# Kernel tuning notes

Hardware: AMD Instinct MI355X
Metric: run time of the kernel (lower is better)

Reference implementation:

```python
import jax, jax.numpy as jnp
import numpy as np
from jax.scipy.special import logsumexp

D_MODEL = 512
NHEAD = 8
BATCH = 2
SEQ = 1024


def _safe_log_relu(v):
    # log(max(v, 0)) with well-defined (zero) gradient where v <= 0
    pos = v > 0
    return jnp.where(pos, jnp.log(jnp.where(pos, v, 1.0)), -jnp.inf)


def _split_heads(t, h):
    b, l, hd = t.shape
    return t.reshape(b, l, h, hd // h).transpose(0, 2, 1, 3)  # (B,H,L,d)


def setup_inputs() -> dict:
    key = jax.random.key(0)
    ks = jax.random.split(key, 9)
    s = 1.0 / np.sqrt(D_MODEL)
    x = jax.random.normal(ks[0], (BATCH, SEQ, D_MODEL), jnp.float32)
    mk = lambda k: jax.random.normal(k, (D_MODEL, D_MODEL), jnp.float32) * s
    mb = lambda k: jax.random.normal(k, (D_MODEL,), jnp.float32) * 0.02
    return {
        "x": x,
        "W_Q": mk(ks[1]), "b_Q": mb(ks[2]),
        "W_K": mk(ks[3]), "b_K": mb(ks[4]),
        "W_V": mk(ks[5]), "b_V": mb(ks[6]),
        "W_O": mk(ks[7]), "b_O": mb(ks[8]),
    }


def reference(x, W_Q, b_Q, W_K, b_K, W_V, b_V, W_O, b_O):
    # self-attention: queries = keys = values = x
    Q = _split_heads(x @ W_Q.T + b_Q, NHEAD)  # (B,H,L,D)
    K = _split_heads(x @ W_K.T + b_K, NHEAD)  # (B,H,L,D)
    V = _split_heads(x @ W_V.T + b_V, NHEAD)  # (B,H,L,Dv)

    # normalizer: log sum_j sum_d exp(Q_id) * exp(K_jd)
    log_B = logsumexp(Q + logsumexp(K, axis=-2, keepdims=True), axis=-1)  # (B,H,L)

    log_V_plus = _safe_log_relu(V)[..., None, :]    # (B,H,L,1,Dv)
    log_V_minus = _safe_log_relu(-V)[..., None, :]  # (B,H,L,1,Dv)

    # reduce over key positions: (B,H,L,D,Dv) -> (B,H,D,Dv)
    lse_KV_plus = logsumexp(K[..., :, :, None] + log_V_plus, axis=-3)
    lse_KV_minus = logsumexp(K[..., :, :, None] + log_V_minus, axis=-3)

    # reduce over feature dim D: (B,H,L,D,Dv) -> (B,H,L,Dv)
    log_A_plus = logsumexp(Q[..., None] + lse_KV_plus[..., None, :, :], axis=-2)
    log_A_minus = logsumexp(Q[..., None] + lse_KV_minus[..., None, :, :], axis=-2)

    heads = jnp.exp(log_A_plus - log_B[..., None]) - jnp.exp(log_A_minus - log_B[..., None])

    b, h, l, dv = heads.shape
    joined = heads.transpose(0, 2, 1, 3).reshape(b, l, h * dv)
    return joined @ W_O.T + b_O
```

## Files before the change

### kernel.cpp

```cpp
#include <hip/hip_runtime.h>
#include <math.h>

#define DM   512
#define NH   8
#define HD   64
#define B_   2
#define L_   1024
#define M_   (B_ * L_)

typedef __attribute__((ext_vector_type(8))) short  bfrag;
typedef __attribute__((ext_vector_type(4))) float  fv4;
typedef __attribute__((ext_vector_type(4))) unsigned short usv4;
typedef __attribute__((ext_vector_type(8))) unsigned short usv8;

__device__ __forceinline__ unsigned short f32_bf16_rne(float f) {
    unsigned u = __float_as_uint(f);
    unsigned r = u + 0x7FFF + ((u >> 16) & 1);
    return (unsigned short)(r >> 16);
}
__device__ __forceinline__ float bf16_f32(unsigned short h) {
    return __uint_as_float(((unsigned)h) << 16);
}

__global__ __launch_bounds__(256) void prep_kernel(
    const float* __restrict__ x,
    const float* __restrict__ Wq, const float* __restrict__ Wk,
    const float* __restrict__ Wv, const float* __restrict__ Wo,
    unsigned short* __restrict__ xh, unsigned short* __restrict__ xl,
    unsigned short* __restrict__ wh, unsigned short* __restrict__ wl) {
    int bid = blockIdx.x;
    const float* src; unsigned short *dh, *dl; size_t off;
    if (bid < 1024) {
        src = x; dh = xh; dl = xl; off = (size_t)bid * 1024;
    } else {
        int wsel = (bid - 1024) >> 8;
        int wb   = (bid - 1024) & 255;
        src = (wsel == 0) ? Wq : (wsel == 1) ? Wk : (wsel == 2) ? Wv : Wo;
        dh = wh + (size_t)wsel * 262144;
        dl = wl + (size_t)wsel * 262144;
        off = (size_t)wb * 1024;
    }
    size_t i = off + (size_t)threadIdx.x * 4;
    float4 v = *(const float4*)(src + i);
    usv4 h, l;
    h.x = f32_bf16_rne(v.x); l.x = f32_bf16_rne(v.x - bf16_f32(h.x));
    h.y = f32_bf16_rne(v.y); l.y = f32_bf16_rne(v.y - bf16_f32(h.y));
    h.z = f32_bf16_rne(v.z); l.z = f32_bf16_rne(v.z - bf16_f32(h.z));
    h.w = f32_bf16_rne(v.w); l.w = f32_bf16_rne(v.w - bf16_f32(h.w));
    *(usv4*)(dh + i) = h;
    *(usv4*)(dl + i) = l;
}

#define TM 128
#define TN 64
#define TK 32
#define LDA 40

__device__ __forceinline__ void mfma_gemm_bf16(
    const unsigned short* __restrict__ Ahg, const unsigned short* __restrict__ Alg,
    const unsigned short* __restrict__ Bhg, const unsigned short* __restrict__ Blg,
    const float* __restrict__ bias, float* __restrict__ C, int do_exp) {
    __shared__ __align__(16) unsigned short Ah[TM * LDA];
    __shared__ __align__(16) unsigned short Al[TM * LDA];
    __shared__ __align__(16) unsigned short Bh[TN * LDA];
    __shared__ __align__(16) unsigned short Bl[TN * LDA];

    const int tid  = threadIdx.x;
    const int wave = tid >> 6, lane = tid & 63;
    const int quad = lane >> 4, r16 = lane & 15;
    const int m0 = blockIdx.y * TM, n0 = blockIdx.x * TN;

    fv4 acc[2][4] = {};

    for (int k0 = 0; k0 < DM; k0 += TK) {
#pragma unroll
        for (int t = 0; t < 2; ++t) {
            int idx = tid + t * 256;
            int row = idx >> 2, ch = (idx & 3) << 3;
            size_t g = (size_t)(m0 + row) * DM + k0 + ch;
            *(usv8*)(Ah + row * LDA + ch) = *(const usv8*)(Ahg + g);
            *(usv8*)(Al + row * LDA + ch) = *(const usv8*)(Alg + g);
        }
        {
            int row = tid >> 2, ch = (tid & 3) << 3;
            size_t g = (size_t)(n0 + row) * DM + k0 + ch;
            *(usv8*)(Bh + row * LDA + ch) = *(const usv8*)(Bhg + g);
            *(usv8*)(Bl + row * LDA + ch) = *(const usv8*)(Blg + g);
        }
        __syncthreads();

        bfrag ah[2], al[2], bh[4], bl[4];
#pragma unroll
        for (int i = 0; i < 2; ++i) {
            int off = (wave * 32 + i * 16 + r16) * LDA + quad * 8;
            ah[i] = *(const bfrag*)(Ah + off);
            al[i] = *(const bfrag*)(Al + off);
        }
#pragma unroll
        for (int j = 0; j < 4; ++j) {
            int off = (j * 16 + r16) * LDA + quad * 8;
            bh[j] = *(const bfrag*)(Bh + off);
            bl[j] = *(const bfrag*)(Bl + off);
        }

#pragma unroll
        for (int i = 0; i < 2; ++i)
#pragma unroll
            for (int j = 0; j < 4; ++j) {
                acc[i][j] = __builtin_amdgcn_mfma_f32_16x16x32_bf16(ah[i], bh[j], acc[i][j], 0, 0, 0);
                acc[i][j] = __builtin_amdgcn_mfma_f32_16x16x32_bf16(ah[i], bl[j], acc[i][j], 0, 0, 0);
                acc[i][j] = __builtin_amdgcn_mfma_f32_16x16x32_bf16(al[i], bh[j], acc[i][j], 0, 0, 0);
            }
        __syncthreads();
    }

#pragma unroll
    for (int j = 0; j < 4; ++j) {
        int n = n0 + j * 16 + r16;
        float bn = bias[n];
#pragma unroll
        for (int i = 0; i < 2; ++i) {
#pragma unroll
            for (int r = 0; r < 4; ++r) {
                int m = m0 + wave * 32 + i * 16 + quad * 4 + r;
                float v = acc[i][j][r] + bn;
                if (do_exp) v = __expf(v);
                C[(size_t)m * DM + n] = v;
            }
        }
    }
}

__global__ __launch_bounds__(256) void gemm_qkv_kernel(
    const unsigned short* __restrict__ xh, const unsigned short* __restrict__ xl,
    const unsigned short* __restrict__ wh, const unsigned short* __restrict__ wl,
    const float* __restrict__ bq, const float* __restrict__ bk, const float* __restrict__ bv,
    float* __restrict__ Qe, float* __restrict__ Ke, float* __restrict__ V) {
    int z = blockIdx.z;
    const float* b = (z == 0) ? bq : (z == 1) ? bk : bv;
    float* C = (z == 0) ? Qe : (z == 1) ? Ke : V;
    mfma_gemm_bf16(xh, xl, wh + (size_t)z * 262144, wl + (size_t)z * 262144,
                   b, C, z < 2);
}

__global__ __launch_bounds__(256) void gemm_out_kernel(
    const unsigned short* __restrict__ jh, const unsigned short* __restrict__ jl,
    const unsigned short* __restrict__ wh, const unsigned short* __restrict__ wl,
    const float* __restrict__ bo, float* __restrict__ C) {
    mfma_gemm_bf16(jh, jl, wh + (size_t)3 * 262144, wl + (size_t)3 * 262144,
                   bo, C, 0);
}

#define JT 64
__global__ __launch_bounds__(256) void kv_stats_kernel(
    const float* __restrict__ Kbuf, const float* __restrict__ Vbuf,
    float* __restrict__ Spart, float* __restrict__ zpart) {
    const int split = blockIdx.x, bh = blockIdx.y;
    const int b = bh >> 3, h = bh & 7;
    const int j0 = split * JT;

    __shared__ float EK[JT][HD + 1];
    __shared__ float VS[JT][HD + 1];

    const int tid = threadIdx.x;
#pragma unroll
    for (int t = 0; t < 4; ++t) {
        int idx = tid + t * 256;
        int r = idx >> 4;
        int c = (idx & 15) << 2;
        size_t row = (size_t)(b * L_ + j0 + r) * DM + h * HD + c;
        float4 kv = *(const float4*)(Kbuf + row);
        EK[r][c + 0] = kv.x; EK[r][c + 1] = kv.y;
        EK[r][c + 2] = kv.z; EK[r][c + 3] = kv.w;
        float4 vv = *(const float4*)(Vbuf + row);
        VS[r][c + 0] = vv.x; VS[r][c + 1] = vv.y;
        VS[r][c + 2] = vv.z; VS[r][c + 3] = vv.w;
    }
    __syncthreads();

    const int tx = tid & 15, ty = tid >> 4;
    float acc[4][4] = {{0.f}};
#pragma unroll 8
    for (int jj = 0; jj < JT; ++jj) {
        float ek[4], vs[4];
#pragma unroll
        for (int i = 0; i < 4; ++i) ek[i] = EK[jj][ty * 4 + i];
#pragma unroll
        for (int j = 0; j < 4; ++j) vs[j] = VS[jj][tx * 4 + j];
#pragma unroll
        for (int i = 0; i < 4; ++i)
#pragma unroll
            for (int j = 0; j < 4; ++j) acc[i][j] += ek[i] * vs[j];
    }

    float* sp = Spart + ((size_t)bh * 16 + split) * (HD * HD);
#pragma unroll
    for (int i = 0; i < 4; ++i) {
        float4 o; o.x = acc[i][0]; o.y = acc[i][1]; o.z = acc[i][2]; o.w = acc[i][3];
        *(float4*)(sp + (ty * 4 + i) * HD + tx * 4) = o;
    }
    if (tid < HD) {
        float z = 0.f;
#pragma unroll 8
        for (int jj = 0; jj < JT; ++jj) z += EK[jj][tid];
        zpart[((size_t)bh * 16 + split) * HD + tid] = z;
    }
}

__global__ __launch_bounds__(256) void heads_kernel(
    const float* __restrict__ Qbuf, const float* __restrict__ Spart,
    const float* __restrict__ zpart,
    unsigned short* __restrict__ jh, unsigned short* __restrict__ jl) {
    const int tileI = blockIdx.x, bh = blockIdx.y;
    const int b = bh >> 3, h = bh & 7;

    __shared__ float S[HD][HD + 1];
    __shared__ float zl[HD];

    const int tid = threadIdx.x;
#pragma unroll
    for (int t = 0; t < 16; ++t) {
        int idx = tid + t * 256;
        float s = 0.f;
        const float* sp = Spart + (size_t)bh * 16 * (HD * HD) + idx;
#pragma unroll
        for (int p = 0; p < 16; ++p) s += sp[(size_t)p * (HD * HD)];
        S[idx >> 6][idx & 63] = s;
    }
    if (tid < HD) {
        float z = 0.f;
        const float* zp = zpart + (size_t)bh * 16 * HD + tid;
#pragma unroll
        for (int p = 0; p < 16; ++p) z += zp[(size_t)p * HD];
        zl[tid] = z;
    }
    __syncthreads();

    const int lane = tid & 63, w = tid >> 6;
#pragma unroll 1
    for (int r = 0; r < 16; ++r) {
        int i = tileI * 64 + w * 16 + r;
        float eq = Qbuf[(size_t)(b * L_ + i) * DM + h * HD + lane];

        float denom = eq * zl[lane];
#pragma unroll
        for (int off = 32; off; off >>= 1) denom += __shfl_xor(denom, off, 64);

        float acc = 0.f;
#pragma unroll
        for (int d = 0; d < HD; ++d) {
            float bq = __shfl(eq, d, 64);
            acc += bq * S[d][lane];
        }
        float val = acc / denom;
        size_t oidx = (size_t)(b * L_ + i) * DM + h * HD + lane;
        unsigned short hh = f32_bf16_rne(val);
        unsigned short ll = f32_bf16_rne(val - bf16_f32(hh));
        jh[oidx] = hh;
        jl[oidx] = ll;
    }
}

extern "C" void kernel_launch(void* const* d_in, const int* in_sizes, int n_in,
                              void* d_out, int out_size, void* d_ws, size_t ws_size,
                              hipStream_t stream) {
    const float* x  = (const float*)d_in[0];
    const float* Wq = (const float*)d_in[1];
    const float* bq = (const float*)d_in[2];
    const float* Wk = (const float*)d_in[3];
    const float* bk = (const float*)d_in[4];
    const float* Wv = (const float*)d_in[5];
    const float* bv = (const float*)d_in[6];
    const float* Wo = (const float*)d_in[7];
    const float* bo = (const float*)d_in[8];
    float* out = (float*)d_out;

    float* f = (float*)d_ws;
    const size_t NQ = (size_t)M_ * DM;
    float* Qe    = f;
    float* Ke    = f + NQ;
    float* V     = f + 2 * NQ;
    float* Spart = f + 3 * NQ;
    float* zpart = f + 4 * NQ;
    unsigned short* u = (unsigned short*)(f + 4 * NQ + 16384);
    unsigned short* xh = u;
    unsigned short* xl = u + NQ;
    unsigned short* wh = u + 2 * NQ;
    unsigned short* wl = u + 3 * NQ;
    unsigned short* jh = u + 4 * NQ;
    unsigned short* jl = u + 5 * NQ;

    prep_kernel<<<2048, 256, 0, stream>>>(x, Wq, Wk, Wv, Wo, xh, xl, wh, wl);

    dim3 gQKV(DM / TN, M_ / TM, 3);
    gemm_qkv_kernel<<<gQKV, 256, 0, stream>>>(xh, xl, wh, wl, bq, bk, bv, Qe, Ke, V);

    kv_stats_kernel<<<dim3(16, 16), 256, 0, stream>>>(Ke, V, Spart, zpart);

    heads_kernel<<<dim3(16, 16), 256, 0, stream>>>(Qe, Spart, zpart, jh, jl);

    dim3 gO(DM / TN, M_ / TM, 1);
    gemm_out_kernel<<<gO, 256, 0, stream>>>(jh, jl, wh, wl, bo, out);
}
```

Baseline: 142.5 us.

## Widen QKV GEMM N-tile and vectorize LDS accesses in stats kernels

After: 146.6 us. 1.03x slower.

```diff
diff --git a/kernel.cpp b/kernel.cpp
--- a/kernel.cpp
+++ b/kernel.cpp
@@ -52,25 +52,28 @@
 }
 
 #define TM 128
-#define TN 64
 #define TK 32
 #define LDA 40
 
+template <int TNv>
 __device__ __forceinline__ void mfma_gemm_bf16(
     const unsigned short* __restrict__ Ahg, const unsigned short* __restrict__ Alg,
     const unsigned short* __restrict__ Bhg, const unsigned short* __restrict__ Blg,
     const float* __restrict__ bias, float* __restrict__ C, int do_exp) {
+    constexpr int NF  = TNv / 16;
+    constexpr int BCH = TNv * 4 / 256;
+
     __shared__ __align__(16) unsigned short Ah[TM * LDA];
     __shared__ __align__(16) unsigned short Al[TM * LDA];
-    __shared__ __align__(16) unsigned short Bh[TN * LDA];
-    __shared__ __align__(16) unsigned short Bl[TN * LDA];
+    __shared__ __align__(16) unsigned short Bh[TNv * LDA];
+    __shared__ __align__(16) unsigned short Bl[TNv * LDA];
 
     const int tid  = threadIdx.x;
     const int wave = tid >> 6, lane = tid & 63;
     const int quad = lane >> 4, r16 = lane & 15;
-    const int m0 = blockIdx.y * TM, n0 = blockIdx.x * TN;
-
-    fv4 acc[2][4] = {};
+    const int m0 = blockIdx.y * TM, n0 = blockIdx.x * TNv;
+
+    fv4 acc[2][NF] = {};
 
     for (int k0 = 0; k0 < DM; k0 += TK) {
 #pragma unroll
@@ -81,15 +84,17 @@
             *(usv8*)(Ah + row * LDA + ch) = *(const usv8*)(Ahg + g);
             *(usv8*)(Al + row * LDA + ch) = *(const usv8*)(Alg + g);
         }
-        {
-            int row = tid >> 2, ch = (tid & 3) << 3;
+#pragma unroll
+        for (int t = 0; t < BCH; ++t) {
+            int idx = tid + t * 256;
+            int row = idx >> 2, ch = (idx & 3) << 3;
             size_t g = (size_t)(n0 + row) * DM + k0 + ch;
             *(usv8*)(Bh + row * LDA + ch) = *(const usv8*)(Bhg + g);
             *(usv8*)(Bl + row * LDA + ch) = *(const usv8*)(Blg + g);
         }
         __syncthreads();
 
-        bfrag ah[2], al[2], bh[4], bl[4];
+        bfrag ah[2], al[2], bh[NF], bl[NF];
 #pragma unroll
         for (int i = 0; i < 2; ++i) {
             int off = (wave * 32 + i * 16 + r16) * LDA + quad * 8;
@@ -97,7 +102,7 @@
             al[i] = *(const bfrag*)(Al + off);
         }
 #pragma unroll
-        for (int j = 0; j < 4; ++j) {
+        for (int j = 0; j < NF; ++j) {
             int off = (j * 16 + r16) * LDA + quad * 8;
             bh[j] = *(const bfrag*)(Bh + off);
             bl[j] = *(const bfrag*)(Bl + off);
@@ -106,7 +111,7 @@
 #pragma unroll
         for (int i = 0; i < 2; ++i)
 #pragma unroll
-            for (int j = 0; j < 4; ++j) {
+            for (int j = 0; j < NF; ++j) {
                 acc[i][j] = __builtin_amdgcn_mfma_f32_16x16x32_bf16(ah[i], bh[j], acc[i][j], 0, 0, 0);
                 acc[i][j] = __builtin_amdgcn_mfma_f32_16x16x32_bf16(ah[i], bl[j], acc[i][j], 0, 0, 0);
                 acc[i][j] = __builtin_amdgcn_mfma_f32_16x16x32_bf16(al[i], bh[j], acc[i][j], 0, 0, 0);
@@ -115,7 +120,7 @@
     }
 
 #pragma unroll
-    for (int j = 0; j < 4; ++j) {
+    for (int j = 0; j < NF; ++j) {
         int n = n0 + j * 16 + r16;
         float bn = bias[n];
 #pragma unroll
@@ -131,7 +136,7 @@
     }
 }
 
-__global__ __launch_bounds__(256) void gemm_qkv_kernel(
+__global__ __launch_bounds__(256, 2) void gemm_qkv_kernel(
     const unsigned short* __restrict__ xh, const unsigned short* __restrict__ xl,
     const unsigned short* __restrict__ wh, const unsigned short* __restrict__ wl,
     const float* __restrict__ bq, const float* __restrict__ bk, const float* __restrict__ bv,
@@ -139,16 +144,16 @@
     int z = blockIdx.z;
     const float* b = (z == 0) ? bq : (z == 1) ? bk : bv;
     float* C = (z == 0) ? Qe : (z == 1) ? Ke : V;
-    mfma_gemm_bf16(xh, xl, wh + (size_t)z * 262144, wl + (size_t)z * 262144,
-                   b, C, z < 2);
+    mfma_gemm_bf16<128>(xh, xl, wh + (size_t)z * 262144, wl + (size_t)z * 262144,
+                        b, C, z < 2);
 }
 
 __global__ __launch_bounds__(256) void gemm_out_kernel(
     const unsigned short* __restrict__ jh, const unsigned short* __restrict__ jl,
     const unsigned short* __restrict__ wh, const unsigned short* __restrict__ wl,
     const float* __restrict__ bo, float* __restrict__ C) {
-    mfma_gemm_bf16(jh, jl, wh + (size_t)3 * 262144, wl + (size_t)3 * 262144,
-                   bo, C, 0);
+    mfma_gemm_bf16<64>(jh, jl, wh + (size_t)3 * 262144, wl + (size_t)3 * 262144,
+                       bo, C, 0);
 }
 
 #define JT 64
@@ -159,8 +164,8 @@
     const int b = bh >> 3, h = bh & 7;
     const int j0 = split * JT;
 
-    __shared__ float EK[JT][HD + 1];
-    __shared__ float VS[JT][HD + 1];
+    __shared__ __align__(16) float EK[JT][HD + 4];
+    __shared__ __align__(16) float VS[JT][HD + 4];
 
     const int tid = threadIdx.x;
 #pragma unroll
@@ -170,11 +175,9 @@
         int c = (idx & 15) << 2;
         size_t row = (size_t)(b * L_ + j0 + r) * DM + h * HD + c;
         float4 kv = *(const float4*)(Kbuf + row);
-        EK[r][c + 0] = kv.x; EK[r][c + 1] = kv.y;
-        EK[r][c + 2] = kv.z; EK[r][c + 3] = kv.w;
+        *(float4*)&EK[r][c] = kv;
         float4 vv = *(const float4*)(Vbuf + row);
-        VS[r][c + 0] = vv.x; VS[r][c + 1] = vv.y;
-        VS[r][c + 2] = vv.z; VS[r][c + 3] = vv.w;
+        *(float4*)&VS[r][c] = vv;
     }
     __syncthreads();
 
@@ -182,15 +185,14 @@
     float acc[4][4] = {{0.f}};
 #pragma unroll 8
     for (int jj = 0; jj < JT; ++jj) {
-        float ek[4], vs[4];
-#pragma unroll
-        for (int i = 0; i < 4; ++i) ek[i] = EK[jj][ty * 4 + i];
-#pragma unroll
-        for (int j = 0; j < 4; ++j) vs[j] = VS[jj][tx * 4 + j];
+        float4 ek = *(const float4*)&EK[jj][ty * 4];
+        float4 vs = *(const float4*)&VS[jj][tx * 4];
+        float e[4] = {ek.x, ek.y, ek.z, ek.w};
+        float v[4] = {vs.x, vs.y, vs.z, vs.w};
 #pragma unroll
         for (int i = 0; i < 4; ++i)
 #pragma unroll
-            for (int j = 0; j < 4; ++j) acc[i][j] += ek[i] * vs[j];
+            for (int j = 0; j < 4; ++j) acc[i][j] += e[i] * v[j];
     }
 
     float* sp = Spart + ((size_t)bh * 16 + split) * (HD * HD);
@@ -214,18 +216,22 @@
     const int tileI = blockIdx.x, bh = blockIdx.y;
     const int b = bh >> 3, h = bh & 7;
 
-    __shared__ float S[HD][HD + 1];
+    __shared__ __align__(16) float S[HD][HD + 4];
     __shared__ float zl[HD];
 
     const int tid = threadIdx.x;
 #pragma unroll
-    for (int t = 0; t < 16; ++t) {
-        int idx = tid + t * 256;
-        float s = 0.f;
-        const float* sp = Spart + (size_t)bh * 16 * (HD * HD) + idx;
-#pragma unroll
-        for (int p = 0; p < 16; ++p) s += sp[(size_t)p * (HD * HD)];
-        S[idx >> 6][idx & 63] = s;
+    for (int t = 0; t < 4; ++t) {
+        int idx4 = tid + t * 256;
+        const float* sp = Spart + (size_t)bh * 16 * (HD * HD) + (size_t)idx4 * 4;
+        float4 s = {0.f, 0.f, 0.f, 0.f};
+#pragma unroll
+        for (int p = 0; p < 16; ++p) {
+            float4 v = *(const float4*)(sp + (size_t)p * (HD * HD));
+            s.x += v.x; s.y += v.y; s.z += v.z; s.w += v.w;
+        }
+        int row = idx4 >> 4, col = (idx4 & 15) << 2;
+        *(float4*)&S[row][col] = s;
     }
     if (tid < HD) {
         float z = 0.f;
@@ -292,13 +298,13 @@
 
     prep_kernel<<<2048, 256, 0, stream>>>(x, Wq, Wk, Wv, Wo, xh, xl, wh, wl);
 
-    dim3 gQKV(DM / TN, M_ / TM, 3);
+    dim3 gQKV(DM / 128, M_ / TM, 3);
     gemm_qkv_kernel<<<gQKV, 256, 0, stream>>>(xh, xl, wh, wl, bq, bk, bv, Qe, Ke, V);
 
     kv_stats_kernel<<<dim3(16, 16), 256, 0, stream>>>(Ke, V, Spart, zpart);
 
     heads_kernel<<<dim3(16, 16), 256, 0, stream>>>(Qe, Spart, zpart, jh, jl);
 
-    dim3 gO(DM / TN, M_ / TM, 1);
+    dim3 gO(DM / 64, M_ / TM, 1);
     gemm_out_kernel<<<gO, 256, 0, stream>>>(jh, jl, wh, wl, bo, out);
 }
```
